# Optimization experiments

Measured on AMD Instinct MI355X. Metric: run time of the kernel, lower is better.

## Reference

```python
import jax, jax.numpy as jnp
import numpy as np

KERNEL_MUL = 2.0
KERNEL_NUM = 5


def setup_inputs() -> dict:
    key = jax.random.key(0)
    k1, k2 = jax.random.split(key)
    source = jax.random.normal(k1, (4096, 256), dtype=jnp.float32)
    target = jax.random.normal(k2, (4096, 256), dtype=jnp.float32)
    return {"source": source, "target": target}


def _mmd(source, target):
    n = source.shape[0]
    m = target.shape[0]
    ns = n + m
    total = jnp.concatenate([source, target], axis=0)  # [ns, D]
    # Pairwise squared L2 distances without the O(ns^2 * D) broadcast tensor:
    # ||x_i - x_j||^2 = ||x_i||^2 + ||x_j||^2 - 2 <x_i, x_j>
    sq = jnp.sum(total * total, axis=1)  # [ns]
    l2 = sq[:, None] + sq[None, :] - 2.0 * (total @ total.T)  # [ns, ns]
    # bandwidth computed on detached data in the original (L2_distance.data)
    bandwidth = jax.lax.stop_gradient(jnp.sum(l2)) / (ns * ns - ns)
    bandwidth = bandwidth / (KERNEL_MUL ** (KERNEL_NUM // 2))
    # multi-bandwidth Gaussian kernel sum (fused single pass over l2)
    kernels = jnp.zeros_like(l2)
    for i in range(KERNEL_NUM):
        kernels = kernels + jnp.exp(-l2 / (bandwidth * KERNEL_MUL ** i))
    xx = jnp.sum(kernels[:n, :n]) / (n * n)
    xy = jnp.sum(kernels[:n, n:]) / (-n * m)
    yx = jnp.sum(kernels[n:, :n]) / (-m * n)
    yy = jnp.sum(kernels[n:, n:]) / (m * m)
    return xx + xy + yx + yy


def reference(source, target):
    return _mmd(source, target)
```

## Files before the change

kernel.cpp:

```cpp
#include <hip/hip_runtime.h>
#include <hip/hip_bf16.h>
#include <stdint.h>

#define NS 8192
#define NHALF 4096
#define DIM 256
#define BLK 128
#define BK 64
#define NTILES (NS / BLK)
#define HALF_TILES (NHALF / BLK)
#define NTRI (NTILES * (NTILES + 1) / 2)
#define PREP_BLOCKS 256

typedef __attribute__((ext_vector_type(8))) short bf16x8;
typedef __attribute__((ext_vector_type(4))) float f32x4;
typedef __attribute__((ext_vector_type(8))) unsigned short u16x8;

#define XB_OFF   0
#define SQ_OFF   (NS * DIM * 2)
#define PART_OFF (SQ_OFF + NS * 4)
#define ACC_OFF  (PART_OFF + PREP_BLOCKS * DIM * 4)
#define C0_OFF   (ACC_OFF + 8)
#define WS_NEED  (C0_OFF + 16)

__device__ __forceinline__ unsigned short f2bf(float f) {
  unsigned int u = __float_as_uint(f);
  u += 0x7fffu + ((u >> 16) & 1u);
  return (unsigned short)(u >> 16);
}
__device__ __forceinline__ float bf2f(unsigned short h) {
  return __uint_as_float(((unsigned int)h) << 16);
}

__global__ __launch_bounds__(256) void mmd_prep(
    const float* __restrict__ src, const float* __restrict__ tgt,
    unsigned short* __restrict__ Xb, float* __restrict__ sq,
    float* __restrict__ partials) {
  int tid = threadIdx.x;
  int lane32 = tid & 31;
  int rgrp = tid >> 5;
  int c = lane32 * 8;
  int rowBase = blockIdx.x * 32;

  float colpart[8];
#pragma unroll
  for (int j = 0; j < 8; ++j) colpart[j] = 0.f;

#pragma unroll
  for (int p = 0; p < 4; ++p) {
    int row = rowBase + p * 8 + rgrp;
    const float* X = (row < NHALF) ? (src + (size_t)row * DIM)
                                   : (tgt + (size_t)(row - NHALF) * DIM);
    float4 v0 = *(const float4*)(X + c);
    float4 v1 = *(const float4*)(X + c + 4);
    float vals[8] = {v0.x, v0.y, v0.z, v0.w, v1.x, v1.y, v1.z, v1.w};
    u16x8 h;
    float s = 0.f;
#pragma unroll
    for (int j = 0; j < 8; ++j) {
      unsigned short b = f2bf(vals[j]);
      h[j] = b;
      float rb = bf2f(b);
      s += rb * rb;
      colpart[j] += rb;
    }
    *(u16x8*)(Xb + (size_t)row * DIM + c) = h;
    for (int o = 16; o > 0; o >>= 1) s += __shfl_down(s, o, 32);
    if (lane32 == 0) sq[row] = s;
  }

  __shared__ float cp[8][DIM];
  *(float4*)&cp[rgrp][c]     = make_float4(colpart[0], colpart[1], colpart[2], colpart[3]);
  *(float4*)&cp[rgrp][c + 4] = make_float4(colpart[4], colpart[5], colpart[6], colpart[7]);
  __syncthreads();
  float s8 = 0.f;
#pragma unroll
  for (int r = 0; r < 8; ++r) s8 += cp[r][tid];
  partials[blockIdx.x * DIM + tid] = s8;
}

__global__ __launch_bounds__(256) void mmd_band(
    const float* __restrict__ partials, const float* __restrict__ sq,
    float* __restrict__ c0out) {
  __shared__ double buf2[DIM];
  __shared__ float buf1[DIM];
  int tid = threadIdx.x;
  float cs = 0.f;
  for (int b = 0; b < PREP_BLOCKS; ++b) cs += partials[b * DIM + tid];
  float s1 = 0.f;
  for (int k = 0; k < NS / DIM; ++k) s1 += sq[k * DIM + tid];
  buf2[tid] = (double)cs * (double)cs;
  buf1[tid] = s1;
  __syncthreads();
  for (int o = 128; o > 0; o >>= 1) {
    if (tid < o) { buf2[tid] += buf2[tid + o]; buf1[tid] += buf1[tid + o]; }
    __syncthreads();
  }
  if (tid == 0) {
    double S1 = (double)buf1[0];
    double S2 = buf2[0];
    double sum_l2 = 2.0 * (double)NS * S1 - 2.0 * S2;
    double bw = sum_l2 / ((double)NS * (double)NS - (double)NS);
    bw = bw / 4.0;
    c0out[0] = (float)(1.4426950408889634 / bw);
  }
}

__global__ __launch_bounds__(256, 2) void mmd_gram(
    const unsigned short* __restrict__ Xb, const float* __restrict__ sq,
    const float* __restrict__ c0p, double* __restrict__ accK) {
  int l = blockIdx.x;
  int bj = (int)((sqrtf(8.f * (float)l + 1.f) - 1.f) * 0.5f);
  while ((bj + 1) * (bj + 2) / 2 <= l) bj++;
  while (bj * (bj + 1) / 2 > l) bj--;
  int bi = l - bj * (bj + 1) / 2;

  __shared__ __align__(16) unsigned short As[BLK * BK];
  __shared__ __align__(16) unsigned short Bs[BLK * BK];
  __shared__ float red[256];
  int tid = threadIdx.x;
  int wave = tid >> 6;
  int lane = tid & 63;
  int rowBase = bi * BLK, colBase = bj * BLK;
  int wr = (wave >> 1) * 64;
  int wc = (wave & 1) * 64;

  f32x4 acc[4][4];
#pragma unroll
  for (int m = 0; m < 4; ++m)
#pragma unroll
    for (int n = 0; n < 4; ++n) acc[m][n] = (f32x4){0.f, 0.f, 0.f, 0.f};

  for (int kt = 0; kt < DIM; kt += BK) {
    __syncthreads();
#pragma unroll
    for (int it = 0; it < 4; ++it) {
      int idx = it * 256 + tid;
      int r = idx >> 3;
      int g = idx & 7;
      int gs = g ^ (r & 7);
      const unsigned short* ga = Xb + (size_t)(rowBase + r) * DIM + kt + gs * 8;
      __builtin_amdgcn_global_load_lds(
          (const __attribute__((address_space(1))) void*)ga,
          (__attribute__((address_space(3))) void*)(As + idx * 8), 16, 0, 0);
      const unsigned short* gb = Xb + (size_t)(colBase + r) * DIM + kt + gs * 8;
      __builtin_amdgcn_global_load_lds(
          (const __attribute__((address_space(1))) void*)gb,
          (__attribute__((address_space(3))) void*)(Bs + idx * 8), 16, 0, 0);
    }
    __syncthreads();

#pragma unroll
    for (int ks = 0; ks < 2; ++ks) {
      bf16x8 af[4], bfr[4];
      int kg = ks * 4 + (lane >> 4);
#pragma unroll
      for (int m = 0; m < 4; ++m) {
        int r = wr + m * 16 + (lane & 15);
        af[m] = *(const bf16x8*)(As + r * BK + (kg ^ (r & 7)) * 8);
      }
#pragma unroll
      for (int n = 0; n < 4; ++n) {
        int r = wc + n * 16 + (lane & 15);
        bfr[n] = *(const bf16x8*)(Bs + r * BK + (kg ^ (r & 7)) * 8);
      }
#pragma unroll
      for (int m = 0; m < 4; ++m)
#pragma unroll
        for (int n = 0; n < 4; ++n)
          acc[m][n] = __builtin_amdgcn_mfma_f32_16x16x32_bf16(
              af[m], bfr[n], acc[m][n], 0, 0, 0);
    }
  }

  float c0 = *c0p;
  float sqr[4][4], sqc[4];
  int r4 = (lane >> 4) * 4;
#pragma unroll
  for (int m = 0; m < 4; ++m)
#pragma unroll
    for (int r = 0; r < 4; ++r)
      sqr[m][r] = sq[rowBase + wr + m * 16 + r4 + r];
#pragma unroll
  for (int n = 0; n < 4; ++n)
    sqc[n] = sq[colBase + wc + n * 16 + (lane & 15)];

  float tsum = 0.f;
#pragma unroll
  for (int m = 0; m < 4; ++m)
#pragma unroll
    for (int n = 0; n < 4; ++n)
#pragma unroll
      for (int r = 0; r < 4; ++r) {
        float l2 = sqr[m][r] + sqc[n] - 2.f * acc[m][n][r];
        float u = l2 * c0;
        float e4 = exp2f(-0.0625f * u);
        float e3 = e4 * e4;
        float e2 = e3 * e3;
        float e1 = e2 * e2;
        float e0 = e1 * e1;
        tsum += ((e4 + e3) + (e2 + e1)) + e0;
      }

  red[tid] = tsum;
  __syncthreads();
  for (int o = 128; o > 0; o >>= 1) {
    if (tid < o) red[tid] += red[tid + o];
    __syncthreads();
  }
  if (tid == 0) {
    float sign = ((bi < HALF_TILES) == (bj < HALF_TILES)) ? 1.f : -1.f;
    float factor = (bi == bj) ? sign : 2.f * sign;
    atomicAdd(accK, (double)(factor * red[0]));
  }
}

__global__ void mmd_final(const double* __restrict__ accK, float* __restrict__ out) {
  out[0] = (float)(accK[0] / ((double)NHALF * (double)NHALF));
}

extern "C" void kernel_launch(void* const* d_in, const int* in_sizes, int n_in,
                              void* d_out, int out_size, void* d_ws, size_t ws_size,
                              hipStream_t stream) {
  if (ws_size < (size_t)WS_NEED) return;
  const float* src = (const float*)d_in[0];
  const float* tgt = (const float*)d_in[1];
  char* ws = (char*)d_ws;
  unsigned short* Xb = (unsigned short*)(ws + XB_OFF);
  float* sq          = (float*)(ws + SQ_OFF);
  float* partials    = (float*)(ws + PART_OFF);
  double* accK       = (double*)(ws + ACC_OFF);
  float* c0          = (float*)(ws + C0_OFF);

  hipMemsetAsync(ws + ACC_OFF, 0, 16, stream);
  mmd_prep<<<PREP_BLOCKS, 256, 0, stream>>>(src, tgt, Xb, sq, partials);
  mmd_band<<<1, 256, 0, stream>>>(partials, sq, c0);
  mmd_gram<<<NTRI, 256, 0, stream>>>(Xb, sq, c0, accK);
  mmd_final<<<1, 1, 0, stream>>>(accK, (float*)d_out);
}
```

Baseline: 67.19 us.

## Fold bandwidth and final kernels into prep/gram via atomics and last-block finalize

Removes the single-block bandwidth kernel and the final scalar kernel. Prep now atomically accumulates column sums and the sum of squared norms, each gram block recomputes the bandwidth constant itself, and the last block to finish (tracked by a counter) writes the output. It also folds the bandwidth scale into the squared-norm terms so the exponent argument is one fma, replaces the shared-memory tree reduction with wave shuffles, and raises launch bounds occupancy to 4. This cuts two kernel launches and serial single-block work, at the cost of float atomics (non-deterministic order) and redundant per-block bandwidth computation.

Measured after the change: 150.9 us. 2.25x slower.

```diff
diff --git a/kernel.cpp b/kernel.cpp
--- a/kernel.cpp
+++ b/kernel.cpp
@@ -18,10 +18,12 @@
 
 #define XB_OFF   0
 #define SQ_OFF   (NS * DIM * 2)
-#define PART_OFF (SQ_OFF + NS * 4)
-#define ACC_OFF  (PART_OFF + PREP_BLOCKS * DIM * 4)
-#define C0_OFF   (ACC_OFF + 8)
-#define WS_NEED  (C0_OFF + 16)
+#define ACC_OFF  (SQ_OFF + NS * 4)
+#define CNT_OFF  (ACC_OFF + 8)
+#define S1_OFF   (ACC_OFF + 12)
+#define CS_OFF   (ACC_OFF + 16)
+#define ZERO_BYTES (16 + DIM * 4)
+#define WS_NEED  (CS_OFF + DIM * 4)
 
 __device__ __forceinline__ unsigned short f2bf(float f) {
   unsigned int u = __float_as_uint(f);
@@ -35,7 +37,7 @@
 __global__ __launch_bounds__(256) void mmd_prep(
     const float* __restrict__ src, const float* __restrict__ tgt,
     unsigned short* __restrict__ Xb, float* __restrict__ sq,
-    float* __restrict__ partials) {
+    float* __restrict__ colsum, float* __restrict__ S1p) {
   int tid = threadIdx.x;
   int lane32 = tid & 31;
   int rgrp = tid >> 5;
@@ -45,6 +47,7 @@
   float colpart[8];
 #pragma unroll
   for (int j = 0; j < 8; ++j) colpart[j] = 0.f;
+  float ssum = 0.f;
 
 #pragma unroll
   for (int p = 0; p < 4; ++p) {
@@ -66,49 +69,32 @@
     }
     *(u16x8*)(Xb + (size_t)row * DIM + c) = h;
     for (int o = 16; o > 0; o >>= 1) s += __shfl_down(s, o, 32);
-    if (lane32 == 0) sq[row] = s;
+    if (lane32 == 0) { sq[row] = s; ssum += s; }
   }
 
   __shared__ float cp[8][DIM];
+  __shared__ float rowsum[8];
   *(float4*)&cp[rgrp][c]     = make_float4(colpart[0], colpart[1], colpart[2], colpart[3]);
   *(float4*)&cp[rgrp][c + 4] = make_float4(colpart[4], colpart[5], colpart[6], colpart[7]);
+  if (lane32 == 0) rowsum[rgrp] = ssum;
   __syncthreads();
   float s8 = 0.f;
 #pragma unroll
   for (int r = 0; r < 8; ++r) s8 += cp[r][tid];
-  partials[blockIdx.x * DIM + tid] = s8;
-}
-
-__global__ __launch_bounds__(256) void mmd_band(
-    const float* __restrict__ partials, const float* __restrict__ sq,
-    float* __restrict__ c0out) {
-  __shared__ double buf2[DIM];
-  __shared__ float buf1[DIM];
-  int tid = threadIdx.x;
-  float cs = 0.f;
-  for (int b = 0; b < PREP_BLOCKS; ++b) cs += partials[b * DIM + tid];
-  float s1 = 0.f;
-  for (int k = 0; k < NS / DIM; ++k) s1 += sq[k * DIM + tid];
-  buf2[tid] = (double)cs * (double)cs;
-  buf1[tid] = s1;
-  __syncthreads();
-  for (int o = 128; o > 0; o >>= 1) {
-    if (tid < o) { buf2[tid] += buf2[tid + o]; buf1[tid] += buf1[tid + o]; }
-    __syncthreads();
-  }
+  atomicAdd(&colsum[tid], s8);
   if (tid == 0) {
-    double S1 = (double)buf1[0];
-    double S2 = buf2[0];
-    double sum_l2 = 2.0 * (double)NS * S1 - 2.0 * S2;
-    double bw = sum_l2 / ((double)NS * (double)NS - (double)NS);
-    bw = bw / 4.0;
-    c0out[0] = (float)(1.4426950408889634 / bw);
-  }
-}
-
-__global__ __launch_bounds__(256, 2) void mmd_gram(
+    float t = 0.f;
+#pragma unroll
+    for (int r = 0; r < 8; ++r) t += rowsum[r];
+    atomicAdd(S1p, t);
+  }
+}
+
+__global__ __launch_bounds__(256, 4) void mmd_gram(
     const unsigned short* __restrict__ Xb, const float* __restrict__ sq,
-    const float* __restrict__ c0p, double* __restrict__ accK) {
+    const float* __restrict__ colsum, const float* __restrict__ S1p,
+    double* __restrict__ accK, unsigned int* __restrict__ cnt,
+    float* __restrict__ out) {
   int l = blockIdx.x;
   int bj = (int)((sqrtf(8.f * (float)l + 1.f) - 1.f) * 0.5f);
   while ((bj + 1) * (bj + 2) / 2 <= l) bj++;
@@ -117,13 +103,27 @@
 
   __shared__ __align__(16) unsigned short As[BLK * BK];
   __shared__ __align__(16) unsigned short Bs[BLK * BK];
-  __shared__ float red[256];
+  __shared__ float red4[4];
   int tid = threadIdx.x;
   int wave = tid >> 6;
   int lane = tid & 63;
   int rowBase = bi * BLK, colBase = bj * BLK;
   int wr = (wave >> 1) * 64;
   int wc = (wave & 1) * 64;
+
+  float s2p = 0.f;
+#pragma unroll
+  for (int i = 0; i < 4; ++i) {
+    float cv = colsum[i * 64 + lane];
+    s2p += cv * cv;
+  }
+#pragma unroll
+  for (int o = 32; o > 0; o >>= 1) s2p += __shfl_xor(s2p, o);
+  float S1 = *S1p;
+  double sum_l2 = 2.0 * (double)NS * (double)S1 - 2.0 * (double)s2p;
+  double bw = sum_l2 / ((double)NS * (double)NS - (double)NS) * 0.25;
+  float cE = (float)(-1.4426950408889634 * 0.0625 / bw);
+  float t2 = -2.f * cE;
 
   f32x4 acc[4][4];
 #pragma unroll
@@ -173,17 +173,16 @@
     }
   }
 
-  float c0 = *c0p;
-  float sqr[4][4], sqc[4];
+  float a_[4][4], b_[4];
   int r4 = (lane >> 4) * 4;
 #pragma unroll
   for (int m = 0; m < 4; ++m)
 #pragma unroll
     for (int r = 0; r < 4; ++r)
-      sqr[m][r] = sq[rowBase + wr + m * 16 + r4 + r];
+      a_[m][r] = cE * sq[rowBase + wr + m * 16 + r4 + r];
 #pragma unroll
   for (int n = 0; n < 4; ++n)
-    sqc[n] = sq[colBase + wc + n * 16 + (lane & 15)];
+    b_[n] = cE * sq[colBase + wc + n * 16 + (lane & 15)];
 
   float tsum = 0.f;
 #pragma unroll
@@ -192,9 +191,8 @@
     for (int n = 0; n < 4; ++n)
 #pragma unroll
       for (int r = 0; r < 4; ++r) {
-        float l2 = sqr[m][r] + sqc[n] - 2.f * acc[m][n][r];
-        float u = l2 * c0;
-        float e4 = exp2f(-0.0625f * u);
+        float arg = fmaf(acc[m][n][r], t2, a_[m][r] + b_[n]);
+        float e4 = exp2f(arg);
         float e3 = e4 * e4;
         float e2 = e3 * e3;
         float e1 = e2 * e2;
@@ -202,21 +200,22 @@
         tsum += ((e4 + e3) + (e2 + e1)) + e0;
       }
 
-  red[tid] = tsum;
+#pragma unroll
+  for (int o = 32; o > 0; o >>= 1) tsum += __shfl_down(tsum, o);
+  if (lane == 0) red4[wave] = tsum;
   __syncthreads();
-  for (int o = 128; o > 0; o >>= 1) {
-    if (tid < o) red[tid] += red[tid + o];
-    __syncthreads();
-  }
   if (tid == 0) {
+    float t = (red4[0] + red4[1]) + (red4[2] + red4[3]);
     float sign = ((bi < HALF_TILES) == (bj < HALF_TILES)) ? 1.f : -1.f;
     float factor = (bi == bj) ? sign : 2.f * sign;
-    atomicAdd(accK, (double)(factor * red[0]));
-  }
-}
-
-__global__ void mmd_final(const double* __restrict__ accK, float* __restrict__ out) {
-  out[0] = (float)(accK[0] / ((double)NHALF * (double)NHALF));
+    atomicAdd(accK, (double)(factor * t));
+    __threadfence();
+    unsigned int prev = atomicAdd(cnt, 1u);
+    if (prev == NTRI - 1) {
+      double tot = atomicAdd(accK, 0.0);
+      out[0] = (float)(tot / ((double)NHALF * (double)NHALF));
+    }
+  }
 }
 
 extern "C" void kernel_launch(void* const* d_in, const int* in_sizes, int n_in,
@@ -228,13 +227,13 @@
   char* ws = (char*)d_ws;
   unsigned short* Xb = (unsigned short*)(ws + XB_OFF);
   float* sq          = (float*)(ws + SQ_OFF);
-  float* partials    = (float*)(ws + PART_OFF);
   double* accK       = (double*)(ws + ACC_OFF);
-  float* c0          = (float*)(ws + C0_OFF);
-
-  hipMemsetAsync(ws + ACC_OFF, 0, 16, stream);
-  mmd_prep<<<PREP_BLOCKS, 256, 0, stream>>>(src, tgt, Xb, sq, partials);
-  mmd_band<<<1, 256, 0, stream>>>(partials, sq, c0);
-  mmd_gram<<<NTRI, 256, 0, stream>>>(Xb, sq, c0, accK);
-  mmd_final<<<1, 1, 0, stream>>>(accK, (float*)d_out);
-}
+  unsigned int* cnt  = (unsigned int*)(ws + CNT_OFF);
+  float* S1p         = (float*)(ws + S1_OFF);
+  float* colsum      = (float*)(ws + CS_OFF);
+
+  hipMemsetAsync(ws + ACC_OFF, 0, ZERO_BYTES, stream);
+  mmd_prep<<<PREP_BLOCKS, 256, 0, stream>>>(src, tgt, Xb, sq, colsum, S1p);
+  mmd_gram<<<NTRI, 256, 0, stream>>>(Xb, sq, colsum, S1p, accK, cnt,
+                                     (float*)d_out);
+}
```

## Use 128x64 rectangular tiles over the upper-triangular Gram with new index mapping

Applied to the files above, without the earlier changes.

Switches the Gram tile from 128x128 to 128x64. Each wave now computes a 32x64 slab, and a new closed-form mapping enumerates the 4160 upper-triangular rectangular tiles, with diagonal detection adapted to the rectangular shape. This gives twice as many blocks and smaller per-thread accumulators, for better load balance and occupancy across CUs. The cost is lower data reuse per tile, more global traffic, and more atomics.

Measured after the change: 87.45 us. 1.3x slower.

```diff
diff --git a/kernel.cpp b/kernel.cpp
--- a/kernel.cpp
+++ b/kernel.cpp
@@ -5,11 +5,14 @@
 #define NS 8192
 #define NHALF 4096
 #define DIM 256
-#define BLK 128
+#define BM 128
+#define BN 64
 #define BK 64
-#define NTILES (NS / BLK)
-#define HALF_TILES (NHALF / BLK)
-#define NTRI (NTILES * (NTILES + 1) / 2)
+#define NMT (NS / BM)
+#define NNT (NS / BN)
+#define HALF_MT (NHALF / BM)
+#define HALF_NT (NHALF / BN)
+#define NTILES_TRI 4160
 #define PREP_BLOCKS 256
 
 typedef __attribute__((ext_vector_type(8))) short bf16x8;
@@ -110,24 +113,23 @@
     const unsigned short* __restrict__ Xb, const float* __restrict__ sq,
     const float* __restrict__ c0p, double* __restrict__ accK) {
   int l = blockIdx.x;
-  int bj = (int)((sqrtf(8.f * (float)l + 1.f) - 1.f) * 0.5f);
-  while ((bj + 1) * (bj + 2) / 2 <= l) bj++;
-  while (bj * (bj + 1) / 2 > l) bj--;
-  int bi = l - bj * (bj + 1) / 2;
-
-  __shared__ __align__(16) unsigned short As[BLK * BK];
-  __shared__ __align__(16) unsigned short Bs[BLK * BK];
+  int bi = (int)((129.f - sqrtf(16641.f - 4.f * (float)l)) * 0.5f);
+  while (bi * (129 - bi) > l) bi--;
+  while ((bi + 1) * (129 - (bi + 1)) <= l) bi++;
+  int bj = 2 * bi + (l - bi * (129 - bi));
+
+  __shared__ __align__(16) unsigned short As[BM * BK];
+  __shared__ __align__(16) unsigned short Bs[BN * BK];
   __shared__ float red[256];
   int tid = threadIdx.x;
   int wave = tid >> 6;
   int lane = tid & 63;
-  int rowBase = bi * BLK, colBase = bj * BLK;
-  int wr = (wave >> 1) * 64;
-  int wc = (wave & 1) * 64;
-
-  f32x4 acc[4][4];
-#pragma unroll
-  for (int m = 0; m < 4; ++m)
+  int rowBase = bi * BM, colBase = bj * BN;
+  int wr = wave * 32;
+
+  f32x4 acc[2][4];
+#pragma unroll
+  for (int m = 0; m < 2; ++m)
 #pragma unroll
     for (int n = 0; n < 4; ++n) acc[m][n] = (f32x4){0.f, 0.f, 0.f, 0.f};
 
@@ -143,6 +145,13 @@
       __builtin_amdgcn_global_load_lds(
           (const __attribute__((address_space(1))) void*)ga,
           (__attribute__((address_space(3))) void*)(As + idx * 8), 16, 0, 0);
+    }
+#pragma unroll
+    for (int it = 0; it < 2; ++it) {
+      int idx = it * 256 + tid;
+      int r = idx >> 3;
+      int g = idx & 7;
+      int gs = g ^ (r & 7);
       const unsigned short* gb = Xb + (size_t)(colBase + r) * DIM + kt + gs * 8;
       __builtin_amdgcn_global_load_lds(
           (const __attribute__((address_space(1))) void*)gb,
@@ -152,20 +161,20 @@
 
 #pragma unroll
     for (int ks = 0; ks < 2; ++ks) {
-      bf16x8 af[4], bfr[4];
+      bf16x8 af[2], bfr[4];
       int kg = ks * 4 + (lane >> 4);
 #pragma unroll
-      for (int m = 0; m < 4; ++m) {
+      for (int m = 0; m < 2; ++m) {
         int r = wr + m * 16 + (lane & 15);
         af[m] = *(const bf16x8*)(As + r * BK + (kg ^ (r & 7)) * 8);
       }
 #pragma unroll
       for (int n = 0; n < 4; ++n) {
-        int r = wc + n * 16 + (lane & 15);
+        int r = n * 16 + (lane & 15);
         bfr[n] = *(const bf16x8*)(Bs + r * BK + (kg ^ (r & 7)) * 8);
       }
 #pragma unroll
-      for (int m = 0; m < 4; ++m)
+      for (int m = 0; m < 2; ++m)
 #pragma unroll
         for (int n = 0; n < 4; ++n)
           acc[m][n] = __builtin_amdgcn_mfma_f32_16x16x32_bf16(
@@ -174,20 +183,20 @@
   }
 
   float c0 = *c0p;
-  float sqr[4][4], sqc[4];
+  float sqr[2][4], sqc[4];
   int r4 = (lane >> 4) * 4;
 #pragma unroll
-  for (int m = 0; m < 4; ++m)
+  for (int m = 0; m < 2; ++m)
 #pragma unroll
     for (int r = 0; r < 4; ++r)
       sqr[m][r] = sq[rowBase + wr + m * 16 + r4 + r];
 #pragma unroll
   for (int n = 0; n < 4; ++n)
-    sqc[n] = sq[colBase + wc + n * 16 + (lane & 15)];
+    sqc[n] = sq[colBase + n * 16 + (lane & 15)];
 
   float tsum = 0.f;
 #pragma unroll
-  for (int m = 0; m < 4; ++m)
+  for (int m = 0; m < 2; ++m)
 #pragma unroll
     for (int n = 0; n < 4; ++n)
 #pragma unroll
@@ -209,8 +218,8 @@
     __syncthreads();
   }
   if (tid == 0) {
-    float sign = ((bi < HALF_TILES) == (bj < HALF_TILES)) ? 1.f : -1.f;
-    float factor = (bi == bj) ? sign : 2.f * sign;
+    float sign = ((bi < HALF_MT) == (bj < HALF_NT)) ? 1.f : -1.f;
+    float factor = (bj < 2 * bi + 2) ? sign : 2.f * sign;
     atomicAdd(accK, (double)(factor * red[0]));
   }
 }
@@ -235,6 +244,6 @@
   hipMemsetAsync(ws + ACC_OFF, 0, 16, stream);
   mmd_prep<<<PREP_BLOCKS, 256, 0, stream>>>(src, tgt, Xb, sq, partials);
   mmd_band<<<1, 256, 0, stream>>>(partials, sq, c0);
-  mmd_gram<<<NTRI, 256, 0, stream>>>(Xb, sq, c0, accK);
+  mmd_gram<<<NTILES_TRI, 256, 0, stream>>>(Xb, sq, c0, accK);
   mmd_final<<<1, 1, 0, stream>>>(accK, (float*)d_out);
 }
```

## Double-buffer LDS tiles in gram kernel and streamline epilogue reduction

Applied to the files above, without the earlier changes.

Splits the shared A/B tiles into two buffers so the next K-slice is loaded with global_load_lds while MFMAs run on the current one, with one barrier per iteration. The exp argument is precomputed as scaled row/column norms plus one FMA on the dot product. The block reduction now uses wave shuffles and a 4-entry shared array instead of a shared-memory tree. LDS usage doubles, which may limit occupancy.

After: 69.65 us. +3.7%, slower.

```diff
diff --git a/kernel.cpp b/kernel.cpp
--- a/kernel.cpp
+++ b/kernel.cpp
@@ -7,6 +7,7 @@
 #define DIM 256
 #define BLK 128
 #define BK 64
+#define NKT (DIM / BK)
 #define NTILES (NS / BLK)
 #define HALF_TILES (NHALF / BLK)
 #define NTRI (NTILES * (NTILES + 1) / 2)
@@ -106,6 +107,26 @@
   }
 }
 
+#define STAGE(KT, BUF)                                                        \
+  {                                                                           \
+    _Pragma("unroll") for (int it = 0; it < 4; ++it) {                        \
+      int idx = it * 256 + tid;                                               \
+      int r = idx >> 3, g = idx & 7, gs = g ^ (r & 7);                        \
+      const unsigned short* ga =                                              \
+          Xb + (size_t)(rowBase + r) * DIM + (KT)*BK + gs * 8;                \
+      __builtin_amdgcn_global_load_lds(                                       \
+          (const __attribute__((address_space(1))) void*)ga,                  \
+          (__attribute__((address_space(3))) void*)(&As[BUF][idx * 8]), 16,   \
+          0, 0);                                                              \
+      const unsigned short* gb =                                              \
+          Xb + (size_t)(colBase + r) * DIM + (KT)*BK + gs * 8;                \
+      __builtin_amdgcn_global_load_lds(                                       \
+          (const __attribute__((address_space(1))) void*)gb,                  \
+          (__attribute__((address_space(3))) void*)(&Bs[BUF][idx * 8]), 16,   \
+          0, 0);                                                              \
+    }                                                                         \
+  }
+
 __global__ __launch_bounds__(256, 2) void mmd_gram(
     const unsigned short* __restrict__ Xb, const float* __restrict__ sq,
     const float* __restrict__ c0p, double* __restrict__ accK) {
@@ -115,9 +136,9 @@
   while (bj * (bj + 1) / 2 > l) bj--;
   int bi = l - bj * (bj + 1) / 2;
 
-  __shared__ __align__(16) unsigned short As[BLK * BK];
-  __shared__ __align__(16) unsigned short Bs[BLK * BK];
-  __shared__ float red[256];
+  __shared__ __align__(16) unsigned short As[2][BLK * BK];
+  __shared__ __align__(16) unsigned short Bs[2][BLK * BK];
+  __shared__ float red4[4];
   int tid = threadIdx.x;
   int wave = tid >> 6;
   int lane = tid & 63;
@@ -131,24 +152,13 @@
 #pragma unroll
     for (int n = 0; n < 4; ++n) acc[m][n] = (f32x4){0.f, 0.f, 0.f, 0.f};
 
-  for (int kt = 0; kt < DIM; kt += BK) {
-    __syncthreads();
-#pragma unroll
-    for (int it = 0; it < 4; ++it) {
-      int idx = it * 256 + tid;
-      int r = idx >> 3;
-      int g = idx & 7;
-      int gs = g ^ (r & 7);
-      const unsigned short* ga = Xb + (size_t)(rowBase + r) * DIM + kt + gs * 8;
-      __builtin_amdgcn_global_load_lds(
-          (const __attribute__((address_space(1))) void*)ga,
-          (__attribute__((address_space(3))) void*)(As + idx * 8), 16, 0, 0);
-      const unsigned short* gb = Xb + (size_t)(colBase + r) * DIM + kt + gs * 8;
-      __builtin_amdgcn_global_load_lds(
-          (const __attribute__((address_space(1))) void*)gb,
-          (__attribute__((address_space(3))) void*)(Bs + idx * 8), 16, 0, 0);
-    }
-    __syncthreads();
+  STAGE(0, 0);
+  __syncthreads();
+
+#pragma unroll
+  for (int kt = 0; kt < NKT; ++kt) {
+    int cur = kt & 1;
+    if (kt < NKT - 1) STAGE(kt + 1, cur ^ 1);
 
 #pragma unroll
     for (int ks = 0; ks < 2; ++ks) {
@@ -157,12 +167,12 @@
 #pragma unroll
       for (int m = 0; m < 4; ++m) {
         int r = wr + m * 16 + (lane & 15);
-        af[m] = *(const bf16x8*)(As + r * BK + (kg ^ (r & 7)) * 8);
+        af[m] = *(const bf16x8*)(&As[cur][r * BK + (kg ^ (r & 7)) * 8]);
       }
 #pragma unroll
       for (int n = 0; n < 4; ++n) {
         int r = wc + n * 16 + (lane & 15);
-        bfr[n] = *(const bf16x8*)(Bs + r * BK + (kg ^ (r & 7)) * 8);
+        bfr[n] = *(const bf16x8*)(&Bs[cur][r * BK + (kg ^ (r & 7)) * 8]);
       }
 #pragma unroll
       for (int m = 0; m < 4; ++m)
@@ -171,19 +181,22 @@
           acc[m][n] = __builtin_amdgcn_mfma_f32_16x16x32_bf16(
               af[m], bfr[n], acc[m][n], 0, 0, 0);
     }
+    __syncthreads();
   }
 
   float c0 = *c0p;
-  float sqr[4][4], sqc[4];
+  float cE = -0.0625f * c0;
+  float t2 = -2.f * cE;
+  float a_[4][4], b_[4];
   int r4 = (lane >> 4) * 4;
 #pragma unroll
   for (int m = 0; m < 4; ++m)
 #pragma unroll
     for (int r = 0; r < 4; ++r)
-      sqr[m][r] = sq[rowBase + wr + m * 16 + r4 + r];
+      a_[m][r] = cE * sq[rowBase + wr + m * 16 + r4 + r];
 #pragma unroll
   for (int n = 0; n < 4; ++n)
-    sqc[n] = sq[colBase + wc + n * 16 + (lane & 15)];
+    b_[n] = cE * sq[colBase + wc + n * 16 + (lane & 15)];
 
   float tsum = 0.f;
 #pragma unroll
@@ -192,9 +205,8 @@
     for (int n = 0; n < 4; ++n)
 #pragma unroll
       for (int r = 0; r < 4; ++r) {
-        float l2 = sqr[m][r] + sqc[n] - 2.f * acc[m][n][r];
-        float u = l2 * c0;
-        float e4 = exp2f(-0.0625f * u);
+        float arg = fmaf(acc[m][n][r], t2, a_[m][r] + b_[n]);
+        float e4 = exp2f(arg);
         float e3 = e4 * e4;
         float e2 = e3 * e3;
         float e1 = e2 * e2;
@@ -202,16 +214,15 @@
         tsum += ((e4 + e3) + (e2 + e1)) + e0;
       }
 
-  red[tid] = tsum;
-  __syncthreads();
-  for (int o = 128; o > 0; o >>= 1) {
-    if (tid < o) red[tid] += red[tid + o];
-    __syncthreads();
-  }
+#pragma unroll
+  for (int o = 32; o > 0; o >>= 1) tsum += __shfl_down(tsum, o);
+  if (lane == 0) red4[wave] = tsum;
+  __syncthreads();
   if (tid == 0) {
+    float t = (red4[0] + red4[1]) + (red4[2] + red4[3]);
     float sign = ((bi < HALF_TILES) == (bj < HALF_TILES)) ? 1.f : -1.f;
     float factor = (bi == bj) ? sign : 2.f * sign;
-    atomicAdd(accK, (double)(factor * red[0]));
+    atomicAdd(accK, (double)(factor * t));
   }
 }
 
```
